# Optimization experiments

Measured on AMD Instinct MI355X. Metric: run time of the kernel, lower is better.

## Reference

```python
import jax, jax.numpy as jnp
import numpy as np

EPS = 1e-5

def _ln(x, g, b):
    m = jnp.mean(x, axis=-1, keepdims=True)
    v = jnp.var(x, axis=-1, keepdims=True)
    return (x - m) * jax.lax.rsqrt(v + EPS) * g + b

def _gelu(x):
    return jax.nn.gelu(x, approximate=False)  # torch nn.GELU default is exact erf

def setup_inputs() -> dict:
    key = jax.random.key(0)
    B, N, D, H = 4, 1024, 128, 12
    HID = H * D
    ks = jax.random.split(key, 16)
    s = lambda k, sh, fan: jax.random.normal(k, sh, jnp.float32) * (fan ** -0.5)
    return {
        "x": jax.random.normal(ks[0], (B, N, D), jnp.float32),
        # project: LN(D) -> Linear(D,HID) -> GELU -> Linear(HID,HID)
        "ln1_g": jnp.ones((D,), jnp.float32), "ln1_b": jnp.zeros((D,), jnp.float32),
        "W1": s(ks[1], (D, HID), D), "b1": jnp.zeros((HID,), jnp.float32),
        "W2": s(ks[2], (HID, HID), HID), "b2": jnp.zeros((HID,), jnp.float32),
        # shared Attention(inc=D, outc=D)
        "aln_g": jnp.ones((D,), jnp.float32), "aln_b": jnp.zeros((D,), jnp.float32),
        "Wqkv": s(ks[3], (D, 3 * D), D), "bqkv": jnp.zeros((3 * D,), jnp.float32),
        "Wl": s(ks[4], (D, D), D), "bl": jnp.zeros((D,), jnp.float32),
        # out_proj: LN(HID) -> Linear(HID, D) -> GELU
        "lno_g": jnp.ones((HID,), jnp.float32), "lno_b": jnp.zeros((HID,), jnp.float32),
        "Wo": s(ks[5], (HID, D), HID), "bo": jnp.zeros((D,), jnp.float32),
    }

def reference(x, ln1_g, ln1_b, W1, b1, W2, b2,
              aln_g, aln_b, Wqkv, bqkv, Wl, bl,
              lno_g, lno_b, Wo, bo):
    B, N, D = x.shape
    # project (dropout is identity in eval mode)
    h = _ln(x, ln1_g, ln1_b)
    h = _gelu(h @ W1 + b1)
    h = h @ W2 + b2                      # [B, N, H*D]
    H = h.shape[-1] // D
    # chunk along last dim into H features of width D; fold heads into batch
    f = h.reshape(B, N, H, D).transpose(0, 2, 1, 3).reshape(B * H, N, D)
    # shared Attention applied to each head-chunk
    a = _ln(f, aln_g, aln_b)
    qkv = a @ Wqkv + bqkv
    q, k, v = jnp.split(qkv, 3, axis=-1)
    scores = jax.nn.softmax(jnp.einsum('bnd,bmd->bnm', q, k) * (D ** -0.5), axis=-1)
    o = jnp.einsum('bnm,bmd->bnd', scores, v)
    o = o @ Wl + bl
    o = _gelu(o + f)                     # [B*H, N, D]
    # concat heads back along last dim
    feats = o.reshape(B, H, N, D).transpose(0, 2, 1, 3).reshape(B, N, H * D)
    out = _gelu(_ln(feats, lno_g, lno_b) @ Wo + bo)
    return out
```

## Files before the change

kernel.cpp:

```cpp
#include <hip/hip_runtime.h>
#include <stdint.h>

typedef unsigned short u16;
typedef __attribute__((ext_vector_type(8))) short short8;
typedef __attribute__((ext_vector_type(4))) float floatx4;

__device__ inline float b2f(u16 u) {
  union { uint32_t i; float f; } x; x.i = ((uint32_t)u) << 16; return x.f;
}
__device__ inline u16 f2b(float f) {
  union { float f; uint32_t i; } x; x.f = f;
  uint32_t r = (x.i + 0x7FFFu + ((x.i >> 16) & 1u)) >> 16;
  return (u16)r;
}
__device__ inline float gelu_f(float v) {
  return 0.5f * v * (1.0f + erff(v * 0.70710678118654752440f));
}

#define MFMA16(a, b, c) __builtin_amdgcn_mfma_f32_16x16x32_bf16((a), (b), (c), 0, 0, 0)

__device__ __forceinline__ void gl2lds16(const u16* g, u16* l) {
  __builtin_amdgcn_global_load_lds(
      (const __attribute__((address_space(1))) uint32_t*)(uintptr_t)g,
      (__attribute__((address_space(3))) uint32_t*)(uint32_t)(uintptr_t)l,
      16, 0, 0);
}

__global__ __launch_bounds__(256)
void tpose_all_kernel(const float* __restrict__ W1, const float* __restrict__ W2,
                      const float* __restrict__ Wqkv, const float* __restrict__ Wl,
                      const float* __restrict__ Wo,
                      u16* __restrict__ w1t, u16* __restrict__ w2t,
                      u16* __restrict__ wqkvt, u16* __restrict__ wlt,
                      u16* __restrict__ wot) {
  int id = blockIdx.x;
  const float* src; u16* dst; int R, C, bx, by;
  if (id < 2304)      { src = W2;   dst = w2t;   R = 1536; C = 1536; bx = (id % 48) * 32; by = (id / 48) * 32; }
  else if (id < 2496) { id -= 2304; src = W1;   dst = w1t;   R = 128;  C = 1536; bx = (id % 48) * 32; by = (id / 48) * 32; }
  else if (id < 2688) { id -= 2496; src = Wo;   dst = wot;   R = 1536; C = 128;  bx = (id % 4) * 32;  by = (id / 4) * 32; }
  else if (id < 2736) { id -= 2688; src = Wqkv; dst = wqkvt; R = 128;  C = 384;  bx = (id % 12) * 32; by = (id / 12) * 32; }
  else                { id -= 2736; src = Wl;   dst = wlt;   R = 128;  C = 128;  bx = (id % 4) * 32;  by = (id / 4) * 32; }
  __shared__ u16 t[32][33];
  int tx = threadIdx.x & 31, ty = threadIdx.x >> 5;
  for (int i = 0; i < 32; i += 8)
    t[ty + i][tx] = f2b(src[(size_t)(by + ty + i) * C + bx + tx]);
  __syncthreads();
  for (int i = 0; i < 32; i += 8)
    dst[(size_t)(bx + ty + i) * R + by + tx] = t[tx][ty + i];
}

__global__ __launch_bounds__(256)
void ln128_f32_kernel(const float* __restrict__ X, const float* __restrict__ g,
                      const float* __restrict__ bb, u16* __restrict__ Y) {
  int tid = threadIdx.x, w = tid >> 6, lane = tid & 63;
  int row = blockIdx.x * 4 + w;
  const float* xr = X + (size_t)row * 128;
  float2 xv = *(const float2*)(xr + lane * 2);
  float x0 = xv.x, x1 = xv.y;
  float s = x0 + x1, s2 = x0 * x0 + x1 * x1;
  for (int m = 1; m < 64; m <<= 1) { s += __shfl_xor(s, m, 64); s2 += __shfl_xor(s2, m, 64); }
  float mean = s * (1.0f / 128.0f);
  float var = s2 * (1.0f / 128.0f) - mean * mean;
  float rstd = 1.0f / sqrtf(var + 1e-5f);
  float2 gv = *(const float2*)(g + lane * 2);
  float2 bv = *(const float2*)(bb + lane * 2);
  float y0 = (x0 - mean) * rstd * gv.x + bv.x;
  float y1 = (x1 - mean) * rstd * gv.y + bv.y;
  *(uint32_t*)(Y + (size_t)row * 128 + lane * 2) =
      (uint32_t)f2b(y0) | ((uint32_t)f2b(y1) << 16);
}

__global__ __launch_bounds__(256)
void ln128_perm_kernel(const u16* __restrict__ X, const float* __restrict__ g,
                       const float* __restrict__ bb, u16* __restrict__ Y) {
  int tid = threadIdx.x, w = tid >> 6, lane = tid & 63;
  int rid = blockIdx.x * 4 + w;
  int bh = rid >> 10, n = rid & 1023;
  int b = bh / 12, h = bh % 12;
  const u16* xr = X + ((size_t)(b * 1024 + n)) * 1536 + h * 128;
  uint32_t u = *(const uint32_t*)(xr + lane * 2);
  float x0 = b2f(u & 0xffff), x1 = b2f(u >> 16);
  float s = x0 + x1, s2 = x0 * x0 + x1 * x1;
  for (int m = 1; m < 64; m <<= 1) { s += __shfl_xor(s, m, 64); s2 += __shfl_xor(s2, m, 64); }
  float mean = s * (1.0f / 128.0f);
  float var = s2 * (1.0f / 128.0f) - mean * mean;
  float rstd = 1.0f / sqrtf(var + 1e-5f);
  float2 gv = *(const float2*)(g + lane * 2);
  float2 bv = *(const float2*)(bb + lane * 2);
  float y0 = (x0 - mean) * rstd * gv.x + bv.x;
  float y1 = (x1 - mean) * rstd * gv.y + bv.y;
  *(uint32_t*)(Y + (size_t)rid * 128 + lane * 2) =
      (uint32_t)f2b(y0) | ((uint32_t)f2b(y1) << 16);
}

__global__ __launch_bounds__(256)
void ln1536_kernel(const u16* __restrict__ X, const float* __restrict__ g,
                   const float* __restrict__ bb, u16* __restrict__ Y) {
  int row = blockIdx.x, tid = threadIdx.x;
  const u16* xr = X + (size_t)row * 1536;
  uint32_t u0 = *(const uint32_t*)(xr + tid * 6);
  uint32_t u1 = *(const uint32_t*)(xr + tid * 6 + 2);
  uint32_t u2 = *(const uint32_t*)(xr + tid * 6 + 4);
  float v[6] = { b2f(u0 & 0xffff), b2f(u0 >> 16), b2f(u1 & 0xffff),
                 b2f(u1 >> 16),    b2f(u2 & 0xffff), b2f(u2 >> 16) };
  float s = 0.f, s2 = 0.f;
  for (int j = 0; j < 6; j++) { s += v[j]; s2 += v[j] * v[j]; }
  for (int m = 1; m < 64; m <<= 1) { s += __shfl_xor(s, m, 64); s2 += __shfl_xor(s2, m, 64); }
  __shared__ float red[8];
  int w = tid >> 6, lane = tid & 63;
  if (lane == 0) { red[w] = s; red[4 + w] = s2; }
  __syncthreads();
  s = red[0] + red[1] + red[2] + red[3];
  s2 = red[4] + red[5] + red[6] + red[7];
  float mean = s * (1.0f / 1536.0f);
  float var = s2 * (1.0f / 1536.0f) - mean * mean;
  float rstd = 1.0f / sqrtf(var + 1e-5f);
  uint32_t o[3];
  for (int p = 0; p < 3; p++) {
    int c = tid * 6 + p * 2;
    float y0 = (v[p * 2] - mean) * rstd * g[c] + bb[c];
    float y1 = (v[p * 2 + 1] - mean) * rstd * g[c + 1] + bb[c + 1];
    o[p] = (uint32_t)f2b(y0) | ((uint32_t)f2b(y1) << 16);
  }
  u16* yr = Y + (size_t)row * 1536 + tid * 6;
  *(uint32_t*)(yr) = o[0];
  *(uint32_t*)(yr + 2) = o[1];
  *(uint32_t*)(yr + 4) = o[2];
}

__global__ __launch_bounds__(256)
void qkv_kernel(const u16* __restrict__ A, const u16* __restrict__ BT,
                const float* __restrict__ bias, u16* __restrict__ qkv,
                u16* __restrict__ vT) {
  const int K = 128;
  __shared__ __align__(16) u16 abuf[128 * 32];
  __shared__ __align__(16) u16 bbuf[128 * 32];
  int tid = threadIdx.x;
  int w = tid >> 6, lane = tid & 63, ln = lane & 15, quad = lane >> 4;
  int bm = blockIdx.x * 128, bn = blockIdx.y * 128;
  int wr = w >> 1, wc = w & 1;
  floatx4 acc[4][4] = {};
  for (int k0 = 0; k0 < K; k0 += 32) {
    __syncthreads();
    for (int rd = 0; rd < 2; rd++) {
      int c = tid + rd * 256;
      int row = c >> 2, col = (c & 3) * 8;
      gl2lds16(A + (size_t)(bm + row) * K + k0 + col, abuf + c * 8);
      gl2lds16(BT + (size_t)(bn + row) * K + k0 + col, bbuf + c * 8);
    }
    __syncthreads();
    short8 af[4], bf[4];
    for (int i = 0; i < 4; i++)
      af[i] = *(const short8*)(abuf + (wr * 64 + i * 16 + ln) * 32 + quad * 8);
    for (int j = 0; j < 4; j++)
      bf[j] = *(const short8*)(bbuf + (wc * 64 + j * 16 + ln) * 32 + quad * 8);
    for (int i = 0; i < 4; i++)
      for (int j = 0; j < 4; j++)
        acc[i][j] = MFMA16(af[i], bf[j], acc[i][j]);
  }
  if (blockIdx.y < 2) {
    for (int i = 0; i < 4; i++) {
      int row0 = bm + wr * 64 + i * 16 + quad * 4;
      for (int j = 0; j < 4; j++) {
        int col = bn + wc * 64 + j * 16 + ln;
        float bv = bias[col];
        for (int r = 0; r < 4; r++)
          qkv[(size_t)(row0 + r) * 256 + col] = f2b(acc[i][j][r] + bv);
      }
    }
  } else {
    int bh = bm >> 10;
    int nb = bm & 1023;
    u16* vp = vT + (size_t)bh * 128 * 1024;
    for (int i = 0; i < 4; i++) {
      int n0 = nb + wr * 64 + i * 16 + quad * 4;
      for (int j = 0; j < 4; j++) {
        int d = wc * 64 + j * 16 + ln;
        float bv = bias[256 + d];
        u16 tmp[4];
        for (int r = 0; r < 4; r++) tmp[r] = f2b(acc[i][j][r] + bv);
        *(uint2*)(vp + (size_t)d * 1024 + n0) = *(const uint2*)tmp;
      }
    }
  }
}

template <int GELU, int RES, typename OUTT>
__global__ __launch_bounds__(256)
void gemm64_kernel(const u16* __restrict__ A, const u16* __restrict__ BT,
                   const float* __restrict__ bias, const u16* __restrict__ res,
                   OUTT* __restrict__ C, int M, int N, int K) {
  __shared__ __align__(16) u16 abuf[64 * 32];
  __shared__ __align__(16) u16 bbuf[128 * 32];
  int tid = threadIdx.x;
  int w = tid >> 6, lane = tid & 63, ln = lane & 15, quad = lane >> 4;
  int bm = blockIdx.x * 64, bn = blockIdx.y * 128;
  floatx4 acc[4][2] = {};
  for (int k0 = 0; k0 < K; k0 += 32) {
    __syncthreads();
    for (int rd = 0; rd < 2; rd++) {
      int c = tid + rd * 256;
      int row = c >> 2, col = (c & 3) * 8;
      gl2lds16(BT + (size_t)(bn + row) * K + k0 + col, bbuf + c * 8);
    }
    {
      int c = tid;
      int row = c >> 2, col = (c & 3) * 8;
      gl2lds16(A + (size_t)(bm + row) * K + k0 + col, abuf + c * 8);
    }
    __syncthreads();
    short8 af[4], bf[2];
    for (int i = 0; i < 4; i++)
      af[i] = *(const short8*)(abuf + (i * 16 + ln) * 32 + quad * 8);
    for (int j = 0; j < 2; j++)
      bf[j] = *(const short8*)(bbuf + (w * 32 + j * 16 + ln) * 32 + quad * 8);
    for (int i = 0; i < 4; i++)
      for (int j = 0; j < 2; j++)
        acc[i][j] = MFMA16(af[i], bf[j], acc[i][j]);
  }
  for (int i = 0; i < 4; i++) {
    int row0 = bm + i * 16 + quad * 4;
    for (int j = 0; j < 2; j++) {
      int col = bn + w * 32 + j * 16 + ln;
      float bv = bias[col];
      for (int r = 0; r < 4; r++) {
        float v = acc[i][j][r] + bv;
        if (RES) v += b2f(res[(size_t)(row0 + r) * N + col]);
        if (GELU) v = gelu_f(v);
        if constexpr (sizeof(OUTT) == 2)
          C[(size_t)(row0 + r) * N + col] = f2b(v);
        else
          C[(size_t)(row0 + r) * N + col] = v;
      }
    }
  }
}

template <int GELU, int RES, typename OUTT>
__global__ __launch_bounds__(256)
void gemm64b_kernel(const u16* __restrict__ A, const u16* __restrict__ BT,
                    const float* __restrict__ bias, const u16* __restrict__ res,
                    OUTT* __restrict__ C, int M, int N, int K) {
  __shared__ __align__(16) u16 abuf[2 * 64 * 32];
  __shared__ __align__(16) u16 bbuf[2 * 128 * 32];
  int tid = threadIdx.x;
  int w = tid >> 6, lane = tid & 63, ln = lane & 15, quad = lane >> 4;
  int bm = blockIdx.x * 64, bn = blockIdx.y * 128;
  floatx4 acc[4][2] = {};
  for (int k0 = 0; k0 < K; k0 += 64) {
    __syncthreads();
    for (int ks = 0; ks < 2; ks++) {
      {
        int c = tid;
        int row = c >> 2, cc = c & 3;
        gl2lds16(A + (size_t)(bm + row) * K + k0 + ks * 32 + cc * 8,
                 abuf + ks * 2048 + c * 8);
      }
      for (int rd = 0; rd < 2; rd++) {
        int c = tid + rd * 256;
        int row = c >> 2, cc = c & 3;
        gl2lds16(BT + (size_t)(bn + row) * K + k0 + ks * 32 + cc * 8,
                 bbuf + ks * 4096 + c * 8);
      }
    }
    __syncthreads();
    short8 af[2][4], bf[2][2];
    for (int ks = 0; ks < 2; ks++) {
      for (int i = 0; i < 4; i++)
        af[ks][i] = *(const short8*)(abuf + ks * 2048 + (i * 16 + ln) * 32 + quad * 8);
      for (int j = 0; j < 2; j++)
        bf[ks][j] = *(const short8*)(bbuf + ks * 4096 + (w * 32 + j * 16 + ln) * 32 + quad * 8);
    }
    for (int i = 0; i < 4; i++)
      for (int j = 0; j < 2; j++) {
        acc[i][j] = MFMA16(af[0][i], bf[0][j], acc[i][j]);
        acc[i][j] = MFMA16(af[1][i], bf[1][j], acc[i][j]);
      }
  }
  for (int i = 0; i < 4; i++) {
    int row0 = bm + i * 16 + quad * 4;
    for (int j = 0; j < 2; j++) {
      int col = bn + w * 32 + j * 16 + ln;
      float bv = bias[col];
      for (int r = 0; r < 4; r++) {
        float v = acc[i][j][r] + bv;
        if (RES) v += b2f(res[(size_t)(row0 + r) * N + col]);
        if (GELU) v = gelu_f(v);
        if constexpr (sizeof(OUTT) == 2)
          C[(size_t)(row0 + r) * N + col] = f2b(v);
        else
          C[(size_t)(row0 + r) * N + col] = v;
      }
    }
  }
}

__global__ __launch_bounds__(256)
void gemmwl_kernel(const u16* __restrict__ A, const u16* __restrict__ BT,
                   const float* __restrict__ bias, const u16* __restrict__ res,
                   u16* __restrict__ feats) {
  const int K = 128;
  __shared__ __align__(16) u16 abuf[64 * 32];
  __shared__ __align__(16) u16 bbuf[128 * 32];
  int tid = threadIdx.x;
  int w = tid >> 6, lane = tid & 63, ln = lane & 15, quad = lane >> 4;
  int bm = blockIdx.x * 64;
  floatx4 acc[4][2] = {};
  for (int k0 = 0; k0 < K; k0 += 32) {
    __syncthreads();
    for (int rd = 0; rd < 2; rd++) {
      int c = tid + rd * 256;
      int row = c >> 2, col = (c & 3) * 8;
      gl2lds16(BT + (size_t)row * K + k0 + col, bbuf + c * 8);
    }
    {
      int c = tid;
      int row = c >> 2, col = (c & 3) * 8;
      gl2lds16(A + (size_t)(bm + row) * K + k0 + col, abuf + c * 8);
    }
    __syncthreads();
    short8 af[4], bf[2];
    for (int i = 0; i < 4; i++)
      af[i] = *(const short8*)(abuf + (i * 16 + ln) * 32 + quad * 8);
    for (int j = 0; j < 2; j++)
      bf[j] = *(const short8*)(bbuf + (w * 32 + j * 16 + ln) * 32 + quad * 8);
    for (int i = 0; i < 4; i++)
      for (int j = 0; j < 2; j++)
        acc[i][j] = MFMA16(af[i], bf[j], acc[i][j]);
  }
  int bh = bm >> 10, nb = bm & 1023;
  int b = bh / 12, hh = bh % 12;
  size_t obase = ((size_t)b * 1024) * 1536 + hh * 128;
  for (int i = 0; i < 4; i++) {
    int n0 = nb + i * 16 + quad * 4;
    for (int j = 0; j < 2; j++) {
      int col = w * 32 + j * 16 + ln;
      float bv = bias[col];
      for (int r = 0; r < 4; r++) {
        size_t idx = obase + (size_t)(n0 + r) * 1536 + col;
        float v = acc[i][j][r] + bv + b2f(res[idx]);
        feats[idx] = f2b(gelu_f(v));
      }
    }
  }
}

__global__ __launch_bounds__(256)
void gemm64_part_kernel(const u16* __restrict__ A, const u16* __restrict__ BT,
                        float* __restrict__ pws, int Kfull, int kspan) {
  __shared__ __align__(16) u16 abuf[64 * 32];
  __shared__ __align__(16) u16 bbuf[128 * 32];
  int tid = threadIdx.x;
  int w = tid >> 6, lane = tid & 63, ln = lane & 15, quad = lane >> 4;
  int bm = blockIdx.x * 64;
  int kbeg = blockIdx.y * kspan, kend = kbeg + kspan;
  float* Cp = pws + (size_t)blockIdx.y * 4096 * 128;
  floatx4 acc[4][2] = {};
  for (int k0 = kbeg; k0 < kend; k0 += 32) {
    __syncthreads();
    for (int rd = 0; rd < 2; rd++) {
      int c = tid + rd * 256;
      int row = c >> 2, col = (c & 3) * 8;
      gl2lds16(BT + (size_t)row * Kfull + k0 + col, bbuf + c * 8);
    }
    {
      int c = tid;
      int row = c >> 2, col = (c & 3) * 8;
      gl2lds16(A + (size_t)(bm + row) * Kfull + k0 + col, abuf + c * 8);
    }
    __syncthreads();
    short8 af[4], bf[2];
    for (int i = 0; i < 4; i++)
      af[i] = *(const short8*)(abuf + (i * 16 + ln) * 32 + quad * 8);
    for (int j = 0; j < 2; j++)
      bf[j] = *(const short8*)(bbuf + (w * 32 + j * 16 + ln) * 32 + quad * 8);
    for (int i = 0; i < 4; i++)
      for (int j = 0; j < 2; j++)
        acc[i][j] = MFMA16(af[i], bf[j], acc[i][j]);
  }
  for (int i = 0; i < 4; i++) {
    int row0 = bm + i * 16 + quad * 4;
    for (int j = 0; j < 2; j++) {
      int col = w * 32 + j * 16 + ln;
      for (int r = 0; r < 4; r++)
        Cp[(size_t)(row0 + r) * 128 + col] = acc[i][j][r];
    }
  }
}

__global__ __launch_bounds__(256)
void combine_wo_kernel(const float* __restrict__ p, const float* __restrict__ bias,
                       float* __restrict__ out) {
  int i = blockIdx.x * 256 + threadIdx.x;
  const int SZ = 4096 * 128;
  float v = p[i] + p[i + SZ] + p[i + 2 * SZ] + p[i + 3 * SZ] + bias[i & 127];
  out[i] = gelu_f(v);
}

__global__ __launch_bounds__(256)
void attn_kernel(const u16* __restrict__ qkv, const u16* __restrict__ vT,
                 u16* __restrict__ obuf) {
  int blk = blockIdx.x;
  int xcd = blk & 7, slot = blk >> 3;
  int bh = xcd * 6 + (slot >> 4);
  int qt = slot & 15;
  int tid = threadIdx.x, w = tid >> 6, lane = tid & 63, ln = lane & 15, quad = lane >> 4;
  __shared__ __align__(16) u16 kbuf[4 * 64 * 32];
  __shared__ __align__(16) u16 vbuf[2 * 128 * 32];
  __shared__ __align__(16) u16 pbuf[4][16 * 72];
  const int rs = 256;
  size_t base = (size_t)bh * 1024 * 256;
  const u16* qp = qkv + base;
  const u16* kp = qkv + base + 128;
  const u16* vp = vT + (size_t)bh * 128 * 1024;

  short8 onesb;
  {
    short v = (ln == 0) ? (short)0x3F80 : (short)0;
    for (int j = 0; j < 8; j++) onesb[j] = v;
  }

  int qrow = qt * 64 + w * 16 + ln;
  short8 qf[4];
  for (int st = 0; st < 4; st++)
    qf[st] = *(const short8*)(qp + (size_t)qrow * rs + st * 32 + quad * 8);

  floatx4 o[9] = {};
  const float K2 = 0.08838834764831845f * 1.4426950408889634f;

  for (int kt = 0; kt < 16; kt++) {
    __syncthreads();
    for (int it = 0; it < 4; it++) {
      int c = it * 256 + tid;
      int st = c >> 8, key = (c >> 2) & 63, cc = c & 3;
      gl2lds16(kp + (size_t)(kt * 64 + key) * rs + st * 32 + cc * 8, kbuf + c * 8);
      int kf = c >> 9, d = (c >> 2) & 127;
      gl2lds16(vp + (size_t)d * 1024 + kt * 64 + kf * 32 + cc * 8, vbuf + c * 8);
    }
    __syncthreads();

    floatx4 s[4] = {};
    for (int t = 0; t < 4; t++)
      for (int st = 0; st < 4; st++) {
        short8 bk = *(const short8*)(kbuf + st * 2048 + (t * 16 + ln) * 32 + quad * 8);
        s[t] = MFMA16(qf[st], bk, s[t]);
      }
    for (int r = 0; r < 4; r++) {
      int prow = (quad * 4 + r) * 72;
      pbuf[w][prow + ln]      = f2b(exp2f(s[0][r] * K2));
      pbuf[w][prow + 16 + ln] = f2b(exp2f(s[1][r] * K2));
      pbuf[w][prow + 32 + ln] = f2b(exp2f(s[2][r] * K2));
      pbuf[w][prow + 48 + ln] = f2b(exp2f(s[3][r] * K2));
    }
    for (int kf = 0; kf < 2; kf++) {
      short8 ap = *(const short8*)(&pbuf[w][ln * 72 + kf * 32 + quad * 8]);
      for (int dt = 0; dt < 8; dt++) {
        short8 bv = *(const short8*)(vbuf + kf * 4096 + (dt * 16 + ln) * 32 + quad * 8);
        o[dt] = MFMA16(ap, bv, o[dt]);
      }
      o[8] = MFMA16(ap, onesb, o[8]);
    }
  }

  for (int r = 0; r < 4; r++) {
    float l = __shfl(o[8][r], lane & 48);
    float inv = 1.0f / l;
    int n = qt * 64 + w * 16 + quad * 4 + r;
    size_t ob = ((size_t)bh * 1024 + n) * 128;
    for (int dt = 0; dt < 8; dt++)
      obuf[ob + dt * 16 + ln] = f2b(o[dt][r] * inv);
  }
}

extern "C" void kernel_launch(void* const* d_in, const int* in_sizes, int n_in,
                              void* d_out, int out_size, void* d_ws, size_t ws_size,
                              hipStream_t stream) {
  (void)in_sizes; (void)n_in; (void)out_size; (void)ws_size;
  const float* x    = (const float*)d_in[0];
  const float* ln1g = (const float*)d_in[1];
  const float* ln1b = (const float*)d_in[2];
  const float* W1   = (const float*)d_in[3];
  const float* b1   = (const float*)d_in[4];
  const float* W2   = (const float*)d_in[5];
  const float* b2   = (const float*)d_in[6];
  const float* alng = (const float*)d_in[7];
  const float* alnb = (const float*)d_in[8];
  const float* Wqkv = (const float*)d_in[9];
  const float* bqkv = (const float*)d_in[10];
  const float* Wl   = (const float*)d_in[11];
  const float* bl   = (const float*)d_in[12];
  const float* lnog = (const float*)d_in[13];
  const float* lnob = (const float*)d_in[14];
  const float* Wo   = (const float*)d_in[15];
  const float* bo   = (const float*)d_in[16];
  float* out = (float*)d_out;

  char* ws = (char*)d_ws;
  size_t off = 0;
  auto alloc = [&](size_t elems) { u16* p = (u16*)(ws + off); off += elems * sizeof(u16); return p; };
  u16* w1t   = alloc((size_t)1536 * 128);
  u16* w2t   = alloc((size_t)1536 * 1536);
  u16* wqkvt = alloc((size_t)384 * 128);
  u16* wlt   = alloc((size_t)128 * 128);
  u16* wot   = alloc((size_t)128 * 1536);
  u16* lnx   = alloc((size_t)4096 * 128);
  u16* h1    = alloc((size_t)4096 * 1536);
  u16* h2    = alloc((size_t)4096 * 1536);
  u16* aln   = alloc((size_t)49152 * 128);
  u16* qkv   = alloc((size_t)49152 * 256);
  u16* obuf  = alloc((size_t)49152 * 128);
  u16* vT = h1;
  u16* feats = aln;
  u16* lnf = qkv;
  float* pws = (float*)h1;

  dim3 T(256);
  tpose_all_kernel<<<dim3(2752), T, 0, stream>>>(W1, W2, Wqkv, Wl, Wo,
                                                 w1t, w2t, wqkvt, wlt, wot);
  ln128_f32_kernel<<<dim3(4096 / 4), T, 0, stream>>>(x, ln1g, ln1b, lnx);
  gemm64_kernel<1, 0, u16><<<dim3(4096 / 64, 1536 / 128), T, 0, stream>>>(
      lnx, w1t, b1, nullptr, h1, 4096, 1536, 128);
  gemm64b_kernel<0, 0, u16><<<dim3(4096 / 64, 1536 / 128), T, 0, stream>>>(
      h1, w2t, b2, nullptr, h2, 4096, 1536, 1536);
  ln128_perm_kernel<<<dim3(49152 / 4), T, 0, stream>>>(h2, alng, alnb, aln);
  qkv_kernel<<<dim3(49152 / 128, 3), T, 0, stream>>>(aln, wqkvt, bqkv, qkv, vT);
  attn_kernel<<<dim3(768), T, 0, stream>>>(qkv, vT, obuf);
  gemmwl_kernel<<<dim3(49152 / 64), T, 0, stream>>>(obuf, wlt, bl, h2, feats);
  ln1536_kernel<<<dim3(4096), T, 0, stream>>>(feats, lnog, lnob, lnf);
  gemm64_part_kernel<<<dim3(4096 / 64, 4), T, 0, stream>>>(lnf, wot, pws, 1536, 384);
  combine_wo_kernel<<<dim3(4096 * 128 / 256), T, 0, stream>>>(pws, bo, out);
}
```

Baseline: 254.0 us.

## Split-K W2 GEMM with 128x128 tiles, fuse reduction into LN-permute, merge prep kernels

Replaces the 64x128-tile W2 GEMM with a 128x128-tile GEMM that splits K into two halves and writes fp32 partial sums. The reduction and bias add move into the head-permuted LayerNorm kernel, which also writes the bf16 h2 residual. The input LayerNorm is folded into the weight transpose kernel, so one launch goes away. The larger tiles give more reuse per load and split-K keeps the grid at 768 blocks, but the fp32 partials add extra write and read traffic. Workspace buffers are reassigned to make room.

```diff
diff --git a/kernel.cpp b/kernel.cpp
--- a/kernel.cpp
+++ b/kernel.cpp
@@ -27,13 +27,34 @@
 }
 
 __global__ __launch_bounds__(256)
-void tpose_all_kernel(const float* __restrict__ W1, const float* __restrict__ W2,
-                      const float* __restrict__ Wqkv, const float* __restrict__ Wl,
-                      const float* __restrict__ Wo,
-                      u16* __restrict__ w1t, u16* __restrict__ w2t,
-                      u16* __restrict__ wqkvt, u16* __restrict__ wlt,
-                      u16* __restrict__ wot) {
+void prep_kernel(const float* __restrict__ W1, const float* __restrict__ W2,
+                 const float* __restrict__ Wqkv, const float* __restrict__ Wl,
+                 const float* __restrict__ Wo,
+                 u16* __restrict__ w1t, u16* __restrict__ w2t,
+                 u16* __restrict__ wqkvt, u16* __restrict__ wlt,
+                 u16* __restrict__ wot,
+                 const float* __restrict__ X, const float* __restrict__ g,
+                 const float* __restrict__ bb, u16* __restrict__ Y) {
   int id = blockIdx.x;
+  if (id >= 2752) {
+    int tid = threadIdx.x, w = tid >> 6, lane = tid & 63;
+    int row = (id - 2752) * 4 + w;
+    const float* xr = X + (size_t)row * 128;
+    float2 xv = *(const float2*)(xr + lane * 2);
+    float x0 = xv.x, x1 = xv.y;
+    float s = x0 + x1, s2 = x0 * x0 + x1 * x1;
+    for (int m = 1; m < 64; m <<= 1) { s += __shfl_xor(s, m, 64); s2 += __shfl_xor(s2, m, 64); }
+    float mean = s * (1.0f / 128.0f);
+    float var = s2 * (1.0f / 128.0f) - mean * mean;
+    float rstd = 1.0f / sqrtf(var + 1e-5f);
+    float2 gv = *(const float2*)(g + lane * 2);
+    float2 bv = *(const float2*)(bb + lane * 2);
+    float y0 = (x0 - mean) * rstd * gv.x + bv.x;
+    float y1 = (x1 - mean) * rstd * gv.y + bv.y;
+    *(uint32_t*)(Y + (size_t)row * 128 + lane * 2) =
+        (uint32_t)f2b(y0) | ((uint32_t)f2b(y1) << 16);
+    return;
+  }
   const float* src; u16* dst; int R, C, bx, by;
   if (id < 2304)      { src = W2;   dst = w2t;   R = 1536; C = 1536; bx = (id % 48) * 32; by = (id / 48) * 32; }
   else if (id < 2496) { id -= 2304; src = W1;   dst = w1t;   R = 128;  C = 1536; bx = (id % 48) * 32; by = (id / 48) * 32; }
@@ -50,36 +71,21 @@
 }
 
 __global__ __launch_bounds__(256)
-void ln128_f32_kernel(const float* __restrict__ X, const float* __restrict__ g,
-                      const float* __restrict__ bb, u16* __restrict__ Y) {
-  int tid = threadIdx.x, w = tid >> 6, lane = tid & 63;
-  int row = blockIdx.x * 4 + w;
-  const float* xr = X + (size_t)row * 128;
-  float2 xv = *(const float2*)(xr + lane * 2);
-  float x0 = xv.x, x1 = xv.y;
-  float s = x0 + x1, s2 = x0 * x0 + x1 * x1;
-  for (int m = 1; m < 64; m <<= 1) { s += __shfl_xor(s, m, 64); s2 += __shfl_xor(s2, m, 64); }
-  float mean = s * (1.0f / 128.0f);
-  float var = s2 * (1.0f / 128.0f) - mean * mean;
-  float rstd = 1.0f / sqrtf(var + 1e-5f);
-  float2 gv = *(const float2*)(g + lane * 2);
-  float2 bv = *(const float2*)(bb + lane * 2);
-  float y0 = (x0 - mean) * rstd * gv.x + bv.x;
-  float y1 = (x1 - mean) * rstd * gv.y + bv.y;
-  *(uint32_t*)(Y + (size_t)row * 128 + lane * 2) =
-      (uint32_t)f2b(y0) | ((uint32_t)f2b(y1) << 16);
-}
-
-__global__ __launch_bounds__(256)
-void ln128_perm_kernel(const u16* __restrict__ X, const float* __restrict__ g,
-                       const float* __restrict__ bb, u16* __restrict__ Y) {
+void lnperm_comb_kernel(const float* __restrict__ pw, const float* __restrict__ b2,
+                        const float* __restrict__ g, const float* __restrict__ bb,
+                        u16* __restrict__ h2, u16* __restrict__ Y) {
+  const size_t SZ = (size_t)4096 * 1536;
   int tid = threadIdx.x, w = tid >> 6, lane = tid & 63;
   int rid = blockIdx.x * 4 + w;
   int bh = rid >> 10, n = rid & 1023;
   int b = bh / 12, h = bh % 12;
-  const u16* xr = X + ((size_t)(b * 1024 + n)) * 1536 + h * 128;
-  uint32_t u = *(const uint32_t*)(xr + lane * 2);
-  float x0 = b2f(u & 0xffff), x1 = b2f(u >> 16);
+  size_t idx = ((size_t)(b * 1024 + n)) * 1536 + h * 128 + lane * 2;
+  float2 p0 = *(const float2*)(pw + idx);
+  float2 p1 = *(const float2*)(pw + SZ + idx);
+  float2 bv2 = *(const float2*)(b2 + h * 128 + lane * 2);
+  float x0 = p0.x + p1.x + bv2.x;
+  float x1 = p0.y + p1.y + bv2.y;
+  *(uint32_t*)(h2 + idx) = (uint32_t)f2b(x0) | ((uint32_t)f2b(x1) << 16);
   float s = x0 + x1, s2 = x0 * x0 + x1 * x1;
   for (int m = 1; m < 64; m <<= 1) { s += __shfl_xor(s, m, 64); s2 += __shfl_xor(s2, m, 64); }
   float mean = s * (1.0f / 128.0f);
@@ -129,6 +135,47 @@
 }
 
 __global__ __launch_bounds__(256)
+void gemm128_part_kernel(const u16* __restrict__ A, const u16* __restrict__ BT,
+                         float* __restrict__ pw) {
+  const int K = 1536, kspan = 768;
+  __shared__ __align__(16) u16 abuf[128 * 32];
+  __shared__ __align__(16) u16 bbuf[128 * 32];
+  int tid = threadIdx.x;
+  int w = tid >> 6, lane = tid & 63, ln = lane & 15, quad = lane >> 4;
+  int bm = blockIdx.x * 128, bn = blockIdx.y * 128;
+  int wr = w >> 1, wc = w & 1;
+  int kbeg = blockIdx.z * kspan, kend = kbeg + kspan;
+  float* Cp = pw + (size_t)blockIdx.z * 4096 * 1536;
+  floatx4 acc[4][4] = {};
+  for (int k0 = kbeg; k0 < kend; k0 += 32) {
+    __syncthreads();
+    for (int rd = 0; rd < 2; rd++) {
+      int c = tid + rd * 256;
+      int row = c >> 2, col = (c & 3) * 8;
+      gl2lds16(A + (size_t)(bm + row) * K + k0 + col, abuf + c * 8);
+      gl2lds16(BT + (size_t)(bn + row) * K + k0 + col, bbuf + c * 8);
+    }
+    __syncthreads();
+    short8 af[4], bf[4];
+    for (int i = 0; i < 4; i++)
+      af[i] = *(const short8*)(abuf + (wr * 64 + i * 16 + ln) * 32 + quad * 8);
+    for (int j = 0; j < 4; j++)
+      bf[j] = *(const short8*)(bbuf + (wc * 64 + j * 16 + ln) * 32 + quad * 8);
+    for (int i = 0; i < 4; i++)
+      for (int j = 0; j < 4; j++)
+        acc[i][j] = MFMA16(af[i], bf[j], acc[i][j]);
+  }
+  for (int i = 0; i < 4; i++) {
+    int row0 = bm + wr * 64 + i * 16 + quad * 4;
+    for (int j = 0; j < 4; j++) {
+      int col = bn + wc * 64 + j * 16 + ln;
+      for (int r = 0; r < 4; r++)
+        Cp[(size_t)(row0 + r) * 1536 + col] = acc[i][j][r];
+    }
+  }
+}
+
+__global__ __launch_bounds__(256)
 void qkv_kernel(const u16* __restrict__ A, const u16* __restrict__ BT,
                 const float* __restrict__ bias, u16* __restrict__ qkv,
                 u16* __restrict__ vT) {
@@ -217,65 +264,6 @@
     for (int i = 0; i < 4; i++)
       for (int j = 0; j < 2; j++)
         acc[i][j] = MFMA16(af[i], bf[j], acc[i][j]);
-  }
-  for (int i = 0; i < 4; i++) {
-    int row0 = bm + i * 16 + quad * 4;
-    for (int j = 0; j < 2; j++) {
-      int col = bn + w * 32 + j * 16 + ln;
-      float bv = bias[col];
-      for (int r = 0; r < 4; r++) {
-        float v = acc[i][j][r] + bv;
-        if (RES) v += b2f(res[(size_t)(row0 + r) * N + col]);
-        if (GELU) v = gelu_f(v);
-        if constexpr (sizeof(OUTT) == 2)
-          C[(size_t)(row0 + r) * N + col] = f2b(v);
-        else
-          C[(size_t)(row0 + r) * N + col] = v;
-      }
-    }
-  }
-}
-
-template <int GELU, int RES, typename OUTT>
-__global__ __launch_bounds__(256)
-void gemm64b_kernel(const u16* __restrict__ A, const u16* __restrict__ BT,
-                    const float* __restrict__ bias, const u16* __restrict__ res,
-                    OUTT* __restrict__ C, int M, int N, int K) {
-  __shared__ __align__(16) u16 abuf[2 * 64 * 32];
-  __shared__ __align__(16) u16 bbuf[2 * 128 * 32];
-  int tid = threadIdx.x;
-  int w = tid >> 6, lane = tid & 63, ln = lane & 15, quad = lane >> 4;
-  int bm = blockIdx.x * 64, bn = blockIdx.y * 128;
-  floatx4 acc[4][2] = {};
-  for (int k0 = 0; k0 < K; k0 += 64) {
-    __syncthreads();
-    for (int ks = 0; ks < 2; ks++) {
-      {
-        int c = tid;
-        int row = c >> 2, cc = c & 3;
-        gl2lds16(A + (size_t)(bm + row) * K + k0 + ks * 32 + cc * 8,
-                 abuf + ks * 2048 + c * 8);
-      }
-      for (int rd = 0; rd < 2; rd++) {
-        int c = tid + rd * 256;
-        int row = c >> 2, cc = c & 3;
-        gl2lds16(BT + (size_t)(bn + row) * K + k0 + ks * 32 + cc * 8,
-                 bbuf + ks * 4096 + c * 8);
-      }
-    }
-    __syncthreads();
-    short8 af[2][4], bf[2][2];
-    for (int ks = 0; ks < 2; ks++) {
-      for (int i = 0; i < 4; i++)
-        af[ks][i] = *(const short8*)(abuf + ks * 2048 + (i * 16 + ln) * 32 + quad * 8);
-      for (int j = 0; j < 2; j++)
-        bf[ks][j] = *(const short8*)(bbuf + ks * 4096 + (w * 32 + j * 16 + ln) * 32 + quad * 8);
-    }
-    for (int i = 0; i < 4; i++)
-      for (int j = 0; j < 2; j++) {
-        acc[i][j] = MFMA16(af[0][i], bf[0][j], acc[i][j]);
-        acc[i][j] = MFMA16(af[1][i], bf[1][j], acc[i][j]);
-      }
   }
   for (int i = 0; i < 4; i++) {
     int row0 = bm + i * 16 + quad * 4;
@@ -504,28 +492,34 @@
   u16* wlt   = alloc((size_t)128 * 128);
   u16* wot   = alloc((size_t)128 * 1536);
   u16* lnx   = alloc((size_t)4096 * 128);
-  u16* h1    = alloc((size_t)4096 * 1536);
-  u16* h2    = alloc((size_t)4096 * 1536);
-  u16* aln   = alloc((size_t)49152 * 128);
-  u16* qkv   = alloc((size_t)49152 * 256);
-  u16* obuf  = alloc((size_t)49152 * 128);
-  u16* vT = h1;
-  u16* feats = aln;
-  u16* lnf = qkv;
-  float* pws = (float*)h1;
+  u16* R0 = alloc((size_t)4096 * 1536);
+  u16* R1 = alloc((size_t)4096 * 1536);
+  u16* R2 = alloc((size_t)4096 * 1536);
+  u16* R3 = alloc((size_t)49152 * 256);
+  u16* R4 = alloc((size_t)4096 * 1536);
+  float* w2p = (float*)R1;
+  u16* h1out = R0;
+  u16* Y     = R0;
+  u16* h2    = R4;
+  u16* qk    = R3;
+  u16* vT    = R1;
+  u16* attno = R2;
+  u16* feats = R1;
+  u16* lnf   = R2;
+  float* pws = (float*)R0;
 
   dim3 T(256);
-  tpose_all_kernel<<<dim3(2752), T, 0, stream>>>(W1, W2, Wqkv, Wl, Wo,
-                                                 w1t, w2t, wqkvt, wlt, wot);
-  ln128_f32_kernel<<<dim3(4096 / 4), T, 0, stream>>>(x, ln1g, ln1b, lnx);
+  prep_kernel<<<dim3(3776), T, 0, stream>>>(W1, W2, Wqkv, Wl, Wo,
+                                            w1t, w2t, wqkvt, wlt, wot,
+                                            x, ln1g, ln1b, lnx);
   gemm64_kernel<1, 0, u16><<<dim3(4096 / 64, 1536 / 128), T, 0, stream>>>(
-      lnx, w1t, b1, nullptr, h1, 4096, 1536, 128);
-  gemm64b_kernel<0, 0, u16><<<dim3(4096 / 64, 1536 / 128), T, 0, stream>>>(
-      h1, w2t, b2, nullptr, h2, 4096, 1536, 1536);
-  ln128_perm_kernel<<<dim3(49152 / 4), T, 0, stream>>>(h2, alng, alnb, aln);
-  qkv_kernel<<<dim3(49152 / 128, 3), T, 0, stream>>>(aln, wqkvt, bqkv, qkv, vT);
-  attn_kernel<<<dim3(768), T, 0, stream>>>(qkv, vT, obuf);
-  gemmwl_kernel<<<dim3(49152 / 64), T, 0, stream>>>(obuf, wlt, bl, h2, feats);
+      lnx, w1t, b1, nullptr, h1out, 4096, 1536, 128);
+  gemm128_part_kernel<<<dim3(4096 / 128, 1536 / 128, 2), T, 0, stream>>>(
+      h1out, w2t, w2p);
+  lnperm_comb_kernel<<<dim3(49152 / 4), T, 0, stream>>>(w2p, b2, alng, alnb, h2, Y);
+  qkv_kernel<<<dim3(49152 / 128, 3), T, 0, stream>>>(Y, wqkvt, bqkv, qk, vT);
+  attn_kernel<<<dim3(768), T, 0, stream>>>(qk, vT, attno);
+  gemmwl_kernel<<<dim3(49152 / 64), T, 0, stream>>>(attno, wlt, bl, h2, feats);
   ln1536_kernel<<<dim3(4096), T, 0, stream>>>(feats, lnog, lnob, lnf);
   gemm64_part_kernel<<<dim3(4096 / 64, 4), T, 0, stream>>>(lnf, wot, pws, 1536, 384);
   combine_wo_kernel<<<dim3(4096 * 128 / 256), T, 0, stream>>>(pws, bo, out);
```

New measurement: 257.0 us. No clear change (+1.2%).
